# Performance work log

Measured on AMD Instinct MI355X. Metric: run time of the kernel, lower is better.

Reference implementation:

```python
import jax, jax.numpy as jnp
import numpy as np

EPS = 1e-5  # torch BatchNorm2d default eps
K = 3       # kernel_size
D = 1       # dilation (== padding)


def setup_inputs() -> dict:
    key = jax.random.key(0)
    k0, k1, k2 = jax.random.split(key, 3)
    N, C, H, W, O = 4, 2048, 32, 32, 256
    return {
        "x": jax.random.normal(k0, (N, C, H, W), jnp.float32),
        "conv_w": jax.random.normal(k1, (K * K, C, K, K), jnp.float32) * 0.01,
        "gamma": jnp.ones((K * K,), jnp.float32),
        "beta": jnp.zeros((K * K,), jnp.float32),
        "weight": jax.random.normal(k2, (O, C, K * K), jnp.float32) * 0.01,
    }


def reference(x, conv_w, gamma, beta, weight):
    n, c, h, w = x.shape
    # --- dynamic-kernel generator: conv (stride 1, pad=dilation) -> BN (train mode) -> softmax over K*K ---
    sigma = jax.lax.conv_general_dilated(
        x, conv_w, window_strides=(1, 1), padding=[(D, D), (D, D)],
        rhs_dilation=(D, D), dimension_numbers=("NCHW", "OIHW", "NCHW"))  # (n, K*K, h, w)
    mean = sigma.mean(axis=(0, 2, 3), keepdims=True)
    var = sigma.var(axis=(0, 2, 3), keepdims=True)  # biased variance, as torch BN uses for normalization
    sigma = (sigma - mean) * jax.lax.rsqrt(var + EPS)
    sigma = sigma * gamma[None, :, None, None] + beta[None, :, None, None]
    sigma = jax.nn.softmax(sigma, axis=1)            # softmax over the K*K kernel positions
    sigma = sigma.reshape(n, K * K, h * w)           # (n, K*K, h*w)
    # --- unfold (im2col), channel-major (C, kh, kw) ordering matching torch F.unfold ---
    patches = jax.lax.conv_general_dilated_patches(
        x, (K, K), (1, 1), [(D, D), (D, D)], rhs_dilation=(D, D),
        dimension_numbers=("NCHW", "OIHW", "NCHW"))  # (n, C*K*K, h, w)
    patches = patches.reshape(n, c, K * K, h * w)     # (n, C, K*K, h*w)
    # --- per-pixel dynamic weighting + learned projection ---
    # out[n,o,m] = sum_{c,l} patches[n,c,l,m] * sigma[n,l,m] * weight[o,c,l]
    out = jnp.einsum("nclm,nlm,ocl->nom", patches, sigma, weight)
    return out.reshape(n, weight.shape[0], h, w)
```

## Files before the change

### kernel.cpp

```cpp
#include <hip/hip_runtime.h>
#include <hip/hip_bf16.h>
#include <stdint.h>

typedef unsigned short u16;
typedef __attribute__((ext_vector_type(8))) short short8;
typedef __attribute__((ext_vector_type(4))) float floatx4;

#define N_IMG 4
#define C_IN  2048
#define HW    1024
#define KK    9
#define O_OUT 256
#define NPIX  4096
#define M_PAD  2560
#define H_ROWS 2432
#define K_DIM  2048
#define BN_EPS 1e-5f

#define OFF_A    0u
#define OFF_XT   10485760u
#define OFF_H    27262976u
#define OFF_SRAW 47185920u
#define OFF_STAT 47333376u

__device__ __forceinline__ u16 f2b(float f) {
    unsigned u = __float_as_uint(f);
    return (u16)((u + 0x7FFFu + ((u >> 16) & 1u)) >> 16);
}

__device__ __forceinline__ void load8f(const float* base, size_t eidx, u16* out) {
    const float* p = base + eidx;
    float4 a = ((const float4*)p)[0];
    float4 b = ((const float4*)p)[1];
    float f[8] = {a.x, a.y, a.z, a.w, b.x, b.y, b.z, b.w};
#pragma unroll
    for (int j = 0; j < 8; ++j) out[j] = f2b(f[j]);
}

__global__ void build_all(const float* __restrict__ x, const float* __restrict__ wgt,
                          const float* __restrict__ cw, u16* __restrict__ xt,
                          u16* __restrict__ A, float* __restrict__ stats) {
    __shared__ __align__(16) u16 lds[9 * 2056];
    int b = blockIdx.x, t = threadIdx.x;
    if (b < 2048) {
        int c0 = (b & 31) * 64, p0 = ((b >> 5) & 15) * 64, n = b >> 9;
        int rp = t >> 3;
        int pv = (t & 7) * 8;
        u16 h0[8], h1[8];
        load8f(x, (size_t)(n * C_IN + c0 + 2 * rp) * HW + p0 + pv, h0);
        load8f(x, (size_t)(n * C_IN + c0 + 2 * rp + 1) * HW + p0 + pv, h1);
        unsigned* l32 = (unsigned*)lds;
#pragma unroll
        for (int j = 0; j < 8; ++j)
            l32[(pv + j) * 35 + rp] = (unsigned)h0[j] | ((unsigned)h1[j] << 16);
        __syncthreads();
        int pr = t >> 3, cq = (t & 7) * 4;
        unsigned o0[4], o1[4];
#pragma unroll
        for (int i = 0; i < 4; ++i) {
            o0[i] = l32[pr * 35 + cq + i];
            o1[i] = l32[(pr + 32) * 35 + cq + i];
        }
        *(uint4*)(xt + (size_t)(n * HW + p0 + pr) * K_DIM + c0 + cq * 2) = *(uint4*)o0;
        *(uint4*)(xt + (size_t)(n * HW + p0 + pr + 32) * K_DIM + c0 + cq * 2) = *(uint4*)o1;
    } else if (b < 2304) {
        int o = b - 2048;
        size_t base = (size_t)o * 18432;
        for (int i = 0; i < 9; ++i) {
            int e0 = (t + i * 256) * 8;
            u16 hv[8];
            load8f(wgt, base + e0, hv);
#pragma unroll
            for (int j = 0; j < 8; ++j) {
                int e = e0 + j;
                int c = e / 9, l = e - c * 9;
                lds[l * 2056 + c] = hv[j];
            }
        }
        __syncthreads();
        for (int l = 0; l < 9; ++l) {
            size_t row = (size_t)l * 256 + o;
            *(uint4*)(A + row * K_DIM + t * 8) = *(const uint4*)&lds[l * 2056 + t * 8];
        }
    } else if (b < 2313) {
        int l = b - 2304;
        size_t base = (size_t)l * 18432;
        for (int i = 0; i < 9; ++i) {
            int e0 = (t + i * 256) * 8;
            u16 hv[8];
            load8f(cw, base + e0, hv);
#pragma unroll
            for (int j = 0; j < 8; ++j) {
                int e = e0 + j;
                int c = e / 9, k = e - c * 9;
                lds[k * 2056 + c] = hv[j];
            }
        }
        __syncthreads();
        for (int k = 0; k < 9; ++k) {
            size_t row = 2304 + (size_t)k * 9 + l;
            *(uint4*)(A + row * K_DIM + t * 8) = *(const uint4*)&lds[k * 2056 + t * 8];
        }
    } else {
        uint4 z = {0, 0, 0, 0};
        uint4* dst = (uint4*)(A + (size_t)2385 * K_DIM);
        for (int i = t; i < (47 * 2048) / 8; i += 256) dst[i] = z;
        if (t < 18) stats[t] = 0.0f;
    }
}

__device__ __forceinline__ void gload_lds16(const void* g, void* l) {
    __builtin_amdgcn_global_load_lds((__attribute__((address_space(1))) void*)(g),
                                     (__attribute__((address_space(3))) void*)(l), 16, 0, 0);
}

#define STG(gbase, ldsarr, bb, hh, kt) do {                                                        \
    gload_lds16((gbase) + (size_t)((hh) * 128 + (w * 2 + 0) * 8) * K_DIM + (size_t)(kt) * 64,      \
                (ldsarr) + (bb) * 16384 + (hh) * 8192 + ldsw);                                     \
    gload_lds16((gbase) + (size_t)((hh) * 128 + (w * 2 + 1) * 8) * K_DIM + (size_t)(kt) * 64,      \
                (ldsarr) + (bb) * 16384 + (hh) * 8192 + ldsw + 512);                               \
} while (0)

#define RD_A(bb, mi, ks) (*(const short8*)(As + (bb) * 16384 + arow + (mi) * 1024 + col[ks]))
#define RD_B(bb, ni, ks) (*(const short8*)(Bs + (bb) * 16384 + brow + (ni) * 1024 + col[ks]))

#define READ_BALL(bb) do {                                                   \
    bq[0][0] = RD_B(bb, 0, 0); bq[1][0] = RD_B(bb, 1, 0);                    \
    bq[2][0] = RD_B(bb, 2, 0); bq[3][0] = RD_B(bb, 3, 0);                    \
    bq[0][1] = RD_B(bb, 0, 1); bq[1][1] = RD_B(bb, 1, 1);                    \
    bq[2][1] = RD_B(bb, 2, 1); bq[3][1] = RD_B(bb, 3, 1);                    \
} while (0)

#define READ_AQ(bb, qd) do {                                                 \
    aq[0][0] = RD_A(bb, 2 * (qd), 0);     aq[1][0] = RD_A(bb, 2 * (qd) + 1, 0); \
    aq[0][1] = RD_A(bb, 2 * (qd), 1);     aq[1][1] = RD_A(bb, 2 * (qd) + 1, 1); \
} while (0)

#define MFMA1(mi, ni, ks) acc[mi][ni] = __builtin_amdgcn_mfma_f32_16x16x32_bf16( \
    aq[(mi) & 1][ks], bq[ni][ks], acc[mi][ni], 0, 0, 0)

#define MFMA_Q(qd) do {                                                                      \
    MFMA1(2*(qd),   0, 0); MFMA1(2*(qd)+1, 0, 0); MFMA1(2*(qd),   1, 0); MFMA1(2*(qd)+1, 1, 0); \
    MFMA1(2*(qd),   2, 0); MFMA1(2*(qd)+1, 2, 0); MFMA1(2*(qd),   3, 0); MFMA1(2*(qd)+1, 3, 0); \
    MFMA1(2*(qd),   0, 1); MFMA1(2*(qd)+1, 0, 1); MFMA1(2*(qd),   1, 1); MFMA1(2*(qd)+1, 1, 1); \
    MFMA1(2*(qd),   2, 1); MFMA1(2*(qd)+1, 2, 1); MFMA1(2*(qd),   3, 1); MFMA1(2*(qd)+1, 3, 1); \
} while (0)

#define FENCE() asm volatile("" ::: "memory")
#define BARRIER() do { FENCE(); __builtin_amdgcn_s_barrier(); FENCE(); } while (0)

#define BAR1_MFMA(qd) do {                                   \
    BARRIER();                                               \
    __builtin_amdgcn_s_setprio(1);                           \
    MFMA_Q(qd);                                              \
    __builtin_amdgcn_s_setprio(0);                           \
} while (0)
#define VMW4() asm volatile("s_waitcnt vmcnt(4)" ::: "memory")
#define VMW0() asm volatile("s_waitcnt vmcnt(0)" ::: "memory")

__global__ __launch_bounds__(512, 2) void gemm_bt(const u16* __restrict__ A,
                                                  const u16* __restrict__ B,
                                                  __hip_bfloat16* __restrict__ C) {
    __shared__ __align__(16) u16 As[2 * 256 * 64];
    __shared__ __align__(16) u16 Bs[2 * 256 * 64];

    int orig = blockIdx.x;
    int wgid = (orig & 7) * 20 + (orig >> 3);
    int mt = wgid % 10, nt = wgid / 10;
    int m0 = mt * 256, n0 = nt * 256;

    int t = threadIdx.x;
    int w = t >> 6, L = t & 63;
    int wm = w >> 2, wn = w & 3;
    int q = L >> 4, lm = L & 15;
    int lr = L >> 3, ls = L & 7;

    int csw = (ls ^ lr) * 8;
    const u16* gA0 = A + (size_t)(m0 + lr) * K_DIM + csw;
    const u16* gB0 = B + (size_t)(n0 + lr) * K_DIM + csw;
    int ldsw = w * 1024;

    int sw = (lm & 7) << 3;
    int arow = (wm * 128 + lm) * 64;
    int brow = (wn * 64 + lm) * 64;
    int col[2] = { (q * 8) ^ sw, (32 + q * 8) ^ sw };

    floatx4 acc[8][4];
    floatx4 z = {0.f, 0.f, 0.f, 0.f};
#pragma unroll
    for (int i = 0; i < 8; ++i)
#pragma unroll
        for (int j = 0; j < 4; ++j) acc[i][j] = z;

    short8 aq[2][2], bq[4][2];

    STG(gA0, As, 0, 0, 0); STG(gA0, As, 0, 1, 0);
    STG(gB0, Bs, 0, 0, 0); STG(gB0, Bs, 0, 1, 0);
    STG(gB0, Bs, 1, 0, 1); STG(gB0, Bs, 1, 1, 1);
    VMW4();
    BARRIER();

    for (int it = 0; it < 15; ++it) {
        int T = 2 * it;
        READ_AQ(0, 0); READ_BALL(0);
        STG(gA0, As, 1, 0, T + 1); STG(gA0, As, 1, 1, T + 1);
        BAR1_MFMA(0);
        BARRIER();
        READ_AQ(0, 1);
        STG(gB0, Bs, 0, 0, T + 2);
        BAR1_MFMA(1);
        READ_AQ(0, 2);
        STG(gB0, Bs, 0, 1, T + 2);
        BAR1_MFMA(2);
        READ_AQ(0, 3);
        BAR1_MFMA(3); VMW4(); BARRIER();
        READ_AQ(1, 0); READ_BALL(1);
        STG(gA0, As, 0, 0, T + 2); STG(gA0, As, 0, 1, T + 2);
        BAR1_MFMA(0);
        BARRIER();
        READ_AQ(1, 1);
        STG(gB0, Bs, 1, 0, T + 3);
        BAR1_MFMA(1);
        READ_AQ(1, 2);
        STG(gB0, Bs, 1, 1, T + 3);
        BAR1_MFMA(2);
        READ_AQ(1, 3);
        BAR1_MFMA(3); VMW4(); BARRIER();
    }

    READ_AQ(0, 0); READ_BALL(0);
    STG(gA0, As, 1, 0, 31); STG(gA0, As, 1, 1, 31);
    BAR1_MFMA(0);
    READ_AQ(0, 1); BAR1_MFMA(1);
    READ_AQ(0, 2); BAR1_MFMA(2);
    READ_AQ(0, 3); BAR1_MFMA(3); VMW0(); BARRIER();
    READ_AQ(1, 0); READ_BALL(1); BAR1_MFMA(0);
    READ_AQ(1, 1); BAR1_MFMA(1);
    READ_AQ(1, 2); BAR1_MFMA(2);
    READ_AQ(1, 3); BAR1_MFMA(3);

    if (m0 + 255 < H_ROWS) {
#pragma unroll
        for (int mi = 0; mi < 8; ++mi) {
            int gm = m0 + wm * 128 + mi * 16 + q * 4;
#pragma unroll
            for (int ni = 0; ni < 4; ++ni) {
                int gn = n0 + wn * 64 + ni * 16 + lm;
#pragma unroll
                for (int r = 0; r < 4; ++r)
                    C[(size_t)(gm + r) * NPIX + gn] = __float2bfloat16(acc[mi][ni][r]);
            }
        }
    } else {
#pragma unroll
        for (int mi = 0; mi < 8; ++mi) {
            int gm = m0 + wm * 128 + mi * 16 + q * 4;
#pragma unroll
            for (int ni = 0; ni < 4; ++ni) {
                int gn = n0 + wn * 64 + ni * 16 + lm;
#pragma unroll
                for (int r = 0; r < 4; ++r) {
                    int row = gm + r;
                    if (row < H_ROWS)
                        C[(size_t)row * NPIX + gn] = __float2bfloat16(acc[mi][ni][r]);
                }
            }
        }
    }
}

__global__ void sigma_stats(const __hip_bfloat16* __restrict__ Hm, float* __restrict__ sraw,
                            float* __restrict__ stats) {
    int b = blockIdx.x;
    int qq = b & 3, nl = b >> 2;
    int n = nl / 9, l = nl - n * 9;
    int t = threadIdx.x;
    int pix = qq * 256 + t;
    int y = pix >> 5, x = pix & 31;
    float v = 0.f;
#pragma unroll
    for (int k = 0; k < 9; ++k) {
        int yy = y + k / 3 - 1, xx = x + (k % 3) - 1;
        if (yy >= 0 && yy < 32 && xx >= 0 && xx < 32)
            v += __bfloat162float(Hm[(size_t)(2304 + k * 9 + l) * NPIX + n * HW + yy * 32 + xx]);
    }
    sraw[(size_t)nl * HW + pix] = v;
    __shared__ float r1[256], r2[256];
    r1[t] = v; r2[t] = v * v;
    __syncthreads();
    for (int s = 128; s > 0; s >>= 1) {
        if (t < s) { r1[t] += r1[t + s]; r2[t] += r2[t + s]; }
        __syncthreads();
    }
    if (t == 0) { atomicAdd(&stats[l], r1[0]); atomicAdd(&stats[9 + l], r2[0]); }
}

__global__ void tail(const __hip_bfloat16* __restrict__ Hm, const float* __restrict__ sraw,
                     const float* __restrict__ stats, const float* __restrict__ gamma,
                     const float* __restrict__ beta, float* __restrict__ out) {
    int b = blockIdx.x;
    int n = b >> 8, rem = b & 255;
    int ph = rem >> 7, og = rem & 127;
    int t = threadIdx.x;
    float mean[9], istd[9], gg[9], bb[9];
#pragma unroll
    for (int l = 0; l < 9; ++l) {
        float m = stats[l] * (1.f / 4096.f);
        float var = stats[9 + l] * (1.f / 4096.f) - m * m;
        mean[l] = m; istd[l] = rsqrtf(var + BN_EPS);
        gg[l] = gamma[l]; bb[l] = beta[l];
    }
    const __hip_bfloat16* hb = Hm + (size_t)(og * 2) * NPIX + (size_t)n * HW;
    float* ob = out + ((size_t)n * 256 + og * 2) * HW;
#pragma unroll
    for (int i = 0; i < 2; ++i) {
        int pix = ph * 512 + i * 256 + t;
        int y = pix >> 5, x = pix & 31;
        float v[9];
        float mx = -1e30f;
#pragma unroll
        for (int l = 0; l < 9; ++l) {
            float tv = (sraw[(size_t)(n * 9 + l) * HW + pix] - mean[l]) * istd[l];
            tv = tv * gg[l] + bb[l];
            v[l] = tv; mx = fmaxf(mx, tv);
        }
        float ssum = 0.f;
#pragma unroll
        for (int l = 0; l < 9; ++l) { v[l] = __expf(v[l] - mx); ssum += v[l]; }
        float inv = 1.f / ssum;
        float acc0 = 0.f, acc1 = 0.f;
#pragma unroll
        for (int l = 0; l < 9; ++l) {
            int dy = l / 3 - 1, dx = l % 3 - 1;
            int yy = y + dy, xx = x + dx;
            if (yy >= 0 && yy < 32 && xx >= 0 && xx < 32) {
                float sv = v[l] * inv;
                size_t hidx = (size_t)(l * 256) * NPIX + (size_t)(pix + dy * 32 + dx);
                acc0 += sv * __bfloat162float(hb[hidx]);
                acc1 += sv * __bfloat162float(hb[hidx + NPIX]);
            }
        }
        ob[pix] = acc0;
        ob[HW + pix] = acc1;
    }
}

extern "C" void kernel_launch(void* const* d_in, const int* in_sizes, int n_in,
                              void* d_out, int out_size, void* d_ws, size_t ws_size,
                              hipStream_t stream) {
    const float* x     = (const float*)d_in[0];
    const float* cw    = (const float*)d_in[1];
    const float* gamma = (const float*)d_in[2];
    const float* beta  = (const float*)d_in[3];
    const float* wgt   = (const float*)d_in[4];

    char* ws = (char*)d_ws;
    u16*   Abuf = (u16*)(ws + OFF_A);
    u16*   XT   = (u16*)(ws + OFF_XT);
    u16*   Hm   = (u16*)(ws + OFF_H);
    float* sraw = (float*)(ws + OFF_SRAW);
    float* stats= (float*)(ws + OFF_STAT);

    build_all<<<2314, 256, 0, stream>>>(x, wgt, cw, XT, Abuf, stats);
    gemm_bt<<<160, 512, 0, stream>>>(Abuf, XT, (__hip_bfloat16*)Hm);
    sigma_stats<<<N_IMG * KK * 4, 256, 0, stream>>>((const __hip_bfloat16*)Hm, sraw, stats);
    tail<<<1024, 256, 0, stream>>>((const __hip_bfloat16*)Hm, sraw, stats, gamma, beta, (float*)d_out);
}
```

Before: 170.9 us.

## Shrink GEMM M tile to 160 rows so the grid fills all CUs

Changes the GEMM tile from 256x256 to 160x256, giving 256 workgroups instead of 160 so every compute unit on the device gets work. The A staging, LDS buffers, accumulator array and MFMA schedule are rewritten for 5 M sub-tiles per wave (pairs plus a single). It trades lower per-block reuse of B tiles and a less balanced MFMA/barrier schedule for better device-wide load balance.

```diff
diff --git a/kernel.cpp b/kernel.cpp
--- a/kernel.cpp
+++ b/kernel.cpp
@@ -114,14 +114,24 @@
                                      (__attribute__((address_space(3))) void*)(l), 16, 0, 0);
 }
 
-#define STG(gbase, ldsarr, bb, hh, kt) do {                                                        \
-    gload_lds16((gbase) + (size_t)((hh) * 128 + (w * 2 + 0) * 8) * K_DIM + (size_t)(kt) * 64,      \
-                (ldsarr) + (bb) * 16384 + (hh) * 8192 + ldsw);                                     \
-    gload_lds16((gbase) + (size_t)((hh) * 128 + (w * 2 + 1) * 8) * K_DIM + (size_t)(kt) * 64,      \
-                (ldsarr) + (bb) * 16384 + (hh) * 8192 + ldsw + 512);                               \
-} while (0)
-
-#define RD_A(bb, mi, ks) (*(const short8*)(As + (bb) * 16384 + arow + (mi) * 1024 + col[ks]))
+#define STG_A(bb, kt) do {                                                                   \
+    gload_lds16(gA0 + (size_t)(w * 8) * K_DIM + (size_t)(kt) * 64,                           \
+                As + (bb) * 10240 + w * 512);                                                \
+    gload_lds16(gA0 + (size_t)((w + 8) * 8) * K_DIM + (size_t)(kt) * 64,                     \
+                As + (bb) * 10240 + (w + 8) * 512);                                          \
+    if (w < 4)                                                                               \
+        gload_lds16(gA0 + (size_t)((w + 16) * 8) * K_DIM + (size_t)(kt) * 64,                \
+                    As + (bb) * 10240 + (w + 16) * 512);                                     \
+} while (0)
+
+#define STG_B(bb, hh, kt) do {                                                               \
+    gload_lds16(gB0 + (size_t)((hh) * 128 + (w * 2 + 0) * 8) * K_DIM + (size_t)(kt) * 64,    \
+                Bs + (bb) * 16384 + (hh) * 8192 + w * 1024);                                 \
+    gload_lds16(gB0 + (size_t)((hh) * 128 + (w * 2 + 1) * 8) * K_DIM + (size_t)(kt) * 64,    \
+                Bs + (bb) * 16384 + (hh) * 8192 + w * 1024 + 512);                           \
+} while (0)
+
+#define RD_A(bb, mi, ks) (*(const short8*)(As + (bb) * 10240 + arow + (mi) * 1024 + col[ks]))
 #define RD_B(bb, ni, ks) (*(const short8*)(Bs + (bb) * 16384 + brow + (ni) * 1024 + col[ks]))
 
 #define READ_BALL(bb) do {                                                   \
@@ -131,28 +141,48 @@
     bq[2][1] = RD_B(bb, 2, 1); bq[3][1] = RD_B(bb, 3, 1);                    \
 } while (0)
 
-#define READ_AQ(bb, qd) do {                                                 \
-    aq[0][0] = RD_A(bb, 2 * (qd), 0);     aq[1][0] = RD_A(bb, 2 * (qd) + 1, 0); \
-    aq[0][1] = RD_A(bb, 2 * (qd), 1);     aq[1][1] = RD_A(bb, 2 * (qd) + 1, 1); \
-} while (0)
-
-#define MFMA1(mi, ni, ks) acc[mi][ni] = __builtin_amdgcn_mfma_f32_16x16x32_bf16( \
-    aq[(mi) & 1][ks], bq[ni][ks], acc[mi][ni], 0, 0, 0)
-
-#define MFMA_Q(qd) do {                                                                      \
-    MFMA1(2*(qd),   0, 0); MFMA1(2*(qd)+1, 0, 0); MFMA1(2*(qd),   1, 0); MFMA1(2*(qd)+1, 1, 0); \
-    MFMA1(2*(qd),   2, 0); MFMA1(2*(qd)+1, 2, 0); MFMA1(2*(qd),   3, 0); MFMA1(2*(qd)+1, 3, 0); \
-    MFMA1(2*(qd),   0, 1); MFMA1(2*(qd)+1, 0, 1); MFMA1(2*(qd),   1, 1); MFMA1(2*(qd)+1, 1, 1); \
-    MFMA1(2*(qd),   2, 1); MFMA1(2*(qd)+1, 2, 1); MFMA1(2*(qd),   3, 1); MFMA1(2*(qd)+1, 3, 1); \
+#define READ_A2(bb, mlo, mhi) do {                                           \
+    aq[0][0] = RD_A(bb, mlo, 0); aq[1][0] = RD_A(bb, mhi, 0);                \
+    aq[0][1] = RD_A(bb, mlo, 1); aq[1][1] = RD_A(bb, mhi, 1);                \
+} while (0)
+
+#define READ_A1(bb, m) do {                                                  \
+    aq[0][0] = RD_A(bb, m, 0); aq[0][1] = RD_A(bb, m, 1);                    \
+} while (0)
+
+#define MF(a, b, c) __builtin_amdgcn_mfma_f32_16x16x32_bf16(a, b, c, 0, 0, 0)
+
+#define MFMA_PAIR(mlo, mhi) do {                                                             \
+    acc[mlo][0] = MF(aq[0][0], bq[0][0], acc[mlo][0]); acc[mhi][0] = MF(aq[1][0], bq[0][0], acc[mhi][0]); \
+    acc[mlo][1] = MF(aq[0][0], bq[1][0], acc[mlo][1]); acc[mhi][1] = MF(aq[1][0], bq[1][0], acc[mhi][1]); \
+    acc[mlo][2] = MF(aq[0][0], bq[2][0], acc[mlo][2]); acc[mhi][2] = MF(aq[1][0], bq[2][0], acc[mhi][2]); \
+    acc[mlo][3] = MF(aq[0][0], bq[3][0], acc[mlo][3]); acc[mhi][3] = MF(aq[1][0], bq[3][0], acc[mhi][3]); \
+    acc[mlo][0] = MF(aq[0][1], bq[0][1], acc[mlo][0]); acc[mhi][0] = MF(aq[1][1], bq[0][1], acc[mhi][0]); \
+    acc[mlo][1] = MF(aq[0][1], bq[1][1], acc[mlo][1]); acc[mhi][1] = MF(aq[1][1], bq[1][1], acc[mhi][1]); \
+    acc[mlo][2] = MF(aq[0][1], bq[2][1], acc[mlo][2]); acc[mhi][2] = MF(aq[1][1], bq[2][1], acc[mhi][2]); \
+    acc[mlo][3] = MF(aq[0][1], bq[3][1], acc[mlo][3]); acc[mhi][3] = MF(aq[1][1], bq[3][1], acc[mhi][3]); \
+} while (0)
+
+#define MFMA_ONE(m) do {                                                                     \
+    acc[m][0] = MF(aq[0][0], bq[0][0], acc[m][0]); acc[m][1] = MF(aq[0][0], bq[1][0], acc[m][1]); \
+    acc[m][2] = MF(aq[0][0], bq[2][0], acc[m][2]); acc[m][3] = MF(aq[0][0], bq[3][0], acc[m][3]); \
+    acc[m][0] = MF(aq[0][1], bq[0][1], acc[m][0]); acc[m][1] = MF(aq[0][1], bq[1][1], acc[m][1]); \
+    acc[m][2] = MF(aq[0][1], bq[2][1], acc[m][2]); acc[m][3] = MF(aq[0][1], bq[3][1], acc[m][3]); \
 } while (0)
 
 #define FENCE() asm volatile("" ::: "memory")
 #define BARRIER() do { FENCE(); __builtin_amdgcn_s_barrier(); FENCE(); } while (0)
 
-#define BAR1_MFMA(qd) do {                                   \
+#define BAR1_PAIR(mlo, mhi) do {                             \
     BARRIER();                                               \
     __builtin_amdgcn_s_setprio(1);                           \
-    MFMA_Q(qd);                                              \
+    MFMA_PAIR(mlo, mhi);                                     \
+    __builtin_amdgcn_s_setprio(0);                           \
+} while (0)
+#define BAR1_ONE(m) do {                                     \
+    BARRIER();                                               \
+    __builtin_amdgcn_s_setprio(1);                           \
+    MFMA_ONE(m);                                             \
     __builtin_amdgcn_s_setprio(0);                           \
 } while (0)
 #define VMW4() asm volatile("s_waitcnt vmcnt(4)" ::: "memory")
@@ -161,13 +191,13 @@
 __global__ __launch_bounds__(512, 2) void gemm_bt(const u16* __restrict__ A,
                                                   const u16* __restrict__ B,
                                                   __hip_bfloat16* __restrict__ C) {
-    __shared__ __align__(16) u16 As[2 * 256 * 64];
+    __shared__ __align__(16) u16 As[2 * 160 * 64];
     __shared__ __align__(16) u16 Bs[2 * 256 * 64];
 
     int orig = blockIdx.x;
-    int wgid = (orig & 7) * 20 + (orig >> 3);
-    int mt = wgid % 10, nt = wgid / 10;
-    int m0 = mt * 256, n0 = nt * 256;
+    int wgid = (orig & 7) * 32 + (orig >> 3);
+    int nt = wgid >> 4, mt = wgid & 15;
+    int m0 = mt * 160, n0 = nt * 256;
 
     int t = threadIdx.x;
     int w = t >> 6, L = t & 63;
@@ -178,71 +208,67 @@
     int csw = (ls ^ lr) * 8;
     const u16* gA0 = A + (size_t)(m0 + lr) * K_DIM + csw;
     const u16* gB0 = B + (size_t)(n0 + lr) * K_DIM + csw;
-    int ldsw = w * 1024;
 
     int sw = (lm & 7) << 3;
-    int arow = (wm * 128 + lm) * 64;
+    int arow = (wm * 80 + lm) * 64;
     int brow = (wn * 64 + lm) * 64;
     int col[2] = { (q * 8) ^ sw, (32 + q * 8) ^ sw };
 
-    floatx4 acc[8][4];
+    floatx4 acc[5][4];
     floatx4 z = {0.f, 0.f, 0.f, 0.f};
 #pragma unroll
-    for (int i = 0; i < 8; ++i)
+    for (int i = 0; i < 5; ++i)
 #pragma unroll
         for (int j = 0; j < 4; ++j) acc[i][j] = z;
 
     short8 aq[2][2], bq[4][2];
 
-    STG(gA0, As, 0, 0, 0); STG(gA0, As, 0, 1, 0);
-    STG(gB0, Bs, 0, 0, 0); STG(gB0, Bs, 0, 1, 0);
-    STG(gB0, Bs, 1, 0, 1); STG(gB0, Bs, 1, 1, 1);
+    STG_A(0, 0);
+    STG_B(0, 0, 0); STG_B(0, 1, 0);
+    STG_B(1, 0, 1); STG_B(1, 1, 1);
     VMW4();
     BARRIER();
 
     for (int it = 0; it < 15; ++it) {
         int T = 2 * it;
-        READ_AQ(0, 0); READ_BALL(0);
-        STG(gA0, As, 1, 0, T + 1); STG(gA0, As, 1, 1, T + 1);
-        BAR1_MFMA(0);
+        READ_A2(0, 0, 1); READ_BALL(0);
+        STG_A(1, T + 1);
+        BAR1_PAIR(0, 1);
         BARRIER();
-        READ_AQ(0, 1);
-        STG(gB0, Bs, 0, 0, T + 2);
-        BAR1_MFMA(1);
-        READ_AQ(0, 2);
-        STG(gB0, Bs, 0, 1, T + 2);
-        BAR1_MFMA(2);
-        READ_AQ(0, 3);
-        BAR1_MFMA(3); VMW4(); BARRIER();
-        READ_AQ(1, 0); READ_BALL(1);
-        STG(gA0, As, 0, 0, T + 2); STG(gA0, As, 0, 1, T + 2);
-        BAR1_MFMA(0);
+        READ_A2(0, 2, 3);
+        STG_B(0, 0, T + 2);
+        BAR1_PAIR(2, 3);
+        READ_A1(0, 4);
+        STG_B(0, 1, T + 2);
+        BAR1_ONE(4);
+        VMW4(); BARRIER();
+        READ_A2(1, 0, 1); READ_BALL(1);
+        STG_A(0, T + 2);
+        BAR1_PAIR(0, 1);
         BARRIER();
-        READ_AQ(1, 1);
-        STG(gB0, Bs, 1, 0, T + 3);
-        BAR1_MFMA(1);
-        READ_AQ(1, 2);
-        STG(gB0, Bs, 1, 1, T + 3);
-        BAR1_MFMA(2);
-        READ_AQ(1, 3);
-        BAR1_MFMA(3); VMW4(); BARRIER();
-    }
-
-    READ_AQ(0, 0); READ_BALL(0);
-    STG(gA0, As, 1, 0, 31); STG(gA0, As, 1, 1, 31);
-    BAR1_MFMA(0);
-    READ_AQ(0, 1); BAR1_MFMA(1);
-    READ_AQ(0, 2); BAR1_MFMA(2);
-    READ_AQ(0, 3); BAR1_MFMA(3); VMW0(); BARRIER();
-    READ_AQ(1, 0); READ_BALL(1); BAR1_MFMA(0);
-    READ_AQ(1, 1); BAR1_MFMA(1);
-    READ_AQ(1, 2); BAR1_MFMA(2);
-    READ_AQ(1, 3); BAR1_MFMA(3);
-
-    if (m0 + 255 < H_ROWS) {
-#pragma unroll
-        for (int mi = 0; mi < 8; ++mi) {
-            int gm = m0 + wm * 128 + mi * 16 + q * 4;
+        READ_A2(1, 2, 3);
+        STG_B(1, 0, T + 3);
+        BAR1_PAIR(2, 3);
+        READ_A1(1, 4);
+        STG_B(1, 1, T + 3);
+        BAR1_ONE(4);
+        VMW4(); BARRIER();
+    }
+
+    READ_A2(0, 0, 1); READ_BALL(0);
+    STG_A(1, 31);
+    BAR1_PAIR(0, 1);
+    READ_A2(0, 2, 3); BAR1_PAIR(2, 3);
+    READ_A1(0, 4);    BAR1_ONE(4);
+    VMW0(); BARRIER();
+    READ_A2(1, 0, 1); READ_BALL(1); BAR1_PAIR(0, 1);
+    READ_A2(1, 2, 3); BAR1_PAIR(2, 3);
+    READ_A1(1, 4);    BAR1_ONE(4);
+
+    if (m0 + 159 < H_ROWS) {
+#pragma unroll
+        for (int mi = 0; mi < 5; ++mi) {
+            int gm = m0 + wm * 80 + mi * 16 + q * 4;
 #pragma unroll
             for (int ni = 0; ni < 4; ++ni) {
                 int gn = n0 + wn * 64 + ni * 16 + lm;
@@ -253,8 +279,8 @@
         }
     } else {
 #pragma unroll
-        for (int mi = 0; mi < 8; ++mi) {
-            int gm = m0 + wm * 128 + mi * 16 + q * 4;
+        for (int mi = 0; mi < 5; ++mi) {
+            int gm = m0 + wm * 80 + mi * 16 + q * 4;
 #pragma unroll
             for (int ni = 0; ni < 4; ++ni) {
                 int gn = n0 + wn * 64 + ni * 16 + lm;
@@ -362,7 +388,7 @@
     float* stats= (float*)(ws + OFF_STAT);
 
     build_all<<<2314, 256, 0, stream>>>(x, wgt, cw, XT, Abuf, stats);
-    gemm_bt<<<160, 512, 0, stream>>>(Abuf, XT, (__hip_bfloat16*)Hm);
+    gemm_bt<<<256, 512, 0, stream>>>(Abuf, XT, (__hip_bfloat16*)Hm);
     sigma_stats<<<N_IMG * KK * 4, 256, 0, stream>>>((const __hip_bfloat16*)Hm, sraw, stats);
     tail<<<1024, 256, 0, stream>>>((const __hip_bfloat16*)Hm, sraw, stats, gamma, beta, (float*)d_out);
 }
```

Result: faster. 159.8 us (-6.5%).
